# Optimization experiments

Hardware: AMD Instinct MI355X
Metric: run time of the kernel (lower is better)

Reference implementation:

```python
import jax, jax.numpy as jnp
import numpy as np

NUM_HEADS = 8
NORM_GROUPS = 32
EPS = 1e-5


def setup_inputs() -> dict:
    key = jax.random.key(0)
    k1, k2, k3 = jax.random.split(key, 3)
    b, c, h, w = 16, 256, 64, 64
    x = jax.random.normal(k1, (b, c, h, w), dtype=jnp.float32)
    gn_w = jnp.ones((c,), dtype=jnp.float32)
    gn_b = jnp.zeros((c,), dtype=jnp.float32)
    # 1x1 convs == channel matmuls; init like torch (kaiming-ish scale)
    w_qkv = jax.random.normal(k2, (3 * c, c), dtype=jnp.float32) / np.sqrt(c)
    w_proj = jax.random.normal(k3, (c, c), dtype=jnp.float32) / np.sqrt(c)
    b_proj = jnp.zeros((c,), dtype=jnp.float32)
    return {"x": x, "gn_w": gn_w, "gn_b": gn_b, "w_qkv": w_qkv,
            "w_proj": w_proj, "b_proj": b_proj}


def reference(x, gn_w, gn_b, w_qkv, w_proj, b_proj):
    b, c, h, w = x.shape
    H = NUM_HEADS
    d = c // H
    n = h * w
    # GroupNorm over (channels_per_group, h, w)
    xg = x.reshape(b, NORM_GROUPS, -1)
    mu = jnp.mean(xg, axis=-1, keepdims=True)
    var = jnp.mean(jnp.square(xg - mu), axis=-1, keepdims=True)
    xn = ((xg - mu) * jax.lax.rsqrt(var + EPS)).reshape(b, c, h, w)
    xn = xn * gn_w[None, :, None, None] + gn_b[None, :, None, None]
    # 1x1 conv -> (b, 3c, h, w); channel layout is (qkv, heads, d)
    qkv = jnp.einsum('oc,bchw->bohw', w_qkv, xn)
    qkv = qkv.reshape(b, 3, H, d, n)
    q, k, v = qkv[:, 0], qkv[:, 1], qkv[:, 2]  # each (b, H, d, n)
    k = jax.nn.softmax(k, axis=-1)
    # linear attention: small (d x d) state per head
    att = jnp.einsum('bhdn,bhen->bhde', k, v)
    out = jnp.einsum('bhde,bhdn->bhen', att, q)  # (b, H, d, n)
    out = out.reshape(b, c, h, w)
    return jnp.einsum('oc,bchw->bohw', w_proj, out) + b_proj[None, :, None, None]
```

## Files before the change

kernel.cpp:

```cpp
#include <hip/hip_runtime.h>
#include <stdint.h>

#define BATCH 16
#define CCH   256
#define NSP   4096

typedef unsigned short u16;
typedef short  short8 __attribute__((ext_vector_type(8)));
typedef float  f32x4  __attribute__((ext_vector_type(4)));

__device__ __forceinline__ float bf2f(u16 h) {
  union { unsigned int u; float f; } x; x.u = ((unsigned int)h) << 16; return x.f;
}
__device__ __forceinline__ u16 f2bf(float f) {
  union { float f; unsigned int u; } x; x.f = f;
  unsigned int r = 0x7fffu + ((x.u >> 16) & 1u);
  return (u16)((x.u + r) >> 16);
}

#define GLB(p) ((__attribute__((address_space(1))) void*)(p))
#define LDSP(p) ((__attribute__((address_space(3))) void*)(p))

__global__ __launch_bounds__(256) void prep_kernel(const float* __restrict__ x,
                                                   const float* __restrict__ wq,
                                                   const float* __restrict__ wp,
                                                   float2* __restrict__ stats,
                                                   float* __restrict__ att4,
                                                   u16* __restrict__ wbf,
                                                   u16* __restrict__ wqT) {
  __shared__ float red[8];
  __shared__ u16 ls[64][72];
  const int blk = blockIdx.x, tid = threadIdx.x;
  if (blk < 512) {
    {
      float* az = att4 + (size_t)blk * 264;
      for (int i = tid; i < 264; i += 256) az[i] = 0.f;
    }
    const float4* xv = (const float4*)(x + (size_t)blk * 32768);
    float s = 0.f, ss = 0.f;
    for (int i = tid; i < 8192; i += 256) {
      float4 u = xv[i];
      s  += u.x + u.y + u.z + u.w;
      ss += u.x * u.x + u.y * u.y + u.z * u.z + u.w * u.w;
    }
#pragma unroll
    for (int off = 32; off > 0; off >>= 1) {
      s  += __shfl_down(s, off);
      ss += __shfl_down(ss, off);
    }
    const int wave = tid >> 6, lane = tid & 63;
    if (lane == 0) { red[wave * 2] = s; red[wave * 2 + 1] = ss; }
    __syncthreads();
    if (tid == 0) {
      const float S  = red[0] + red[2] + red[4] + red[6];
      const float SS = red[1] + red[3] + red[5] + red[7];
      const float mean = S * (1.f / 32768.f);
      const float var  = SS * (1.f / 32768.f) - mean * mean;
      stats[blk] = make_float2(mean, rsqrtf(var + 1e-5f));
    }
  } else if (blk < 768) {
    const int i = ((blk - 512) * 256 + tid) * 4;
    float4 v = (i < 196608) ? *(const float4*)(wq + i)
                            : *(const float4*)(wp + (i - 196608));
    ushort4 o;
    o.x = f2bf(v.x); o.y = f2bf(v.y); o.z = f2bf(v.z); o.w = f2bf(v.w);
    *(ushort4*)(wbf + i) = o;
  } else {
    const int t2 = blk - 768;
    const int c0 = (t2 & 3) * 64, r0 = (t2 >> 2) * 64;
#pragma unroll
    for (int j = 0; j < 4; ++j) {
      const int row = j * 16 + (tid >> 4), col = (tid & 15) * 4;
      float4 u = *(const float4*)(wq + (r0 + row) * 256 + c0 + col);
      ls[row][col]     = f2bf(u.x);
      ls[row][col + 1] = f2bf(u.y);
      ls[row][col + 2] = f2bf(u.z);
      ls[row][col + 3] = f2bf(u.w);
    }
    __syncthreads();
#pragma unroll
    for (int j = 0; j < 2; ++j) {
      const int crow = j * 32 + (tid >> 3), d8 = (tid & 7) * 8;
      u16 tmp[8];
#pragma unroll
      for (int k = 0; k < 8; ++k) tmp[k] = ls[d8 + k][crow];
      *(uint4*)(wqT + (c0 + crow) * 256 + r0 + d8) = *(uint4*)tmp;
    }
  }
}

__global__ __launch_bounds__(256) void gn_apply_t(const float* __restrict__ x,
                                                  const float* __restrict__ gw,
                                                  const float* __restrict__ gb,
                                                  const float2* __restrict__ stats,
                                                  u16* __restrict__ xnT) {
  __shared__ u16 ls[64][72];
  const int b = blockIdx.z, c0 = blockIdx.y * 64, n0 = blockIdx.x * 64;
  const int tid = threadIdx.x;
#pragma unroll
  for (int r = 0; r < 4; ++r) {
    const int cc = (tid >> 4) + r * 16;
    const int nn = (tid & 15) * 4;
    const int c = c0 + cc;
    const float2 st = stats[b * 32 + (c >> 3)];
    const float wv = gw[c] * st.y;
    const float bv = gb[c] - st.x * wv;
    float4 u = *(const float4*)(x + ((size_t)b * CCH + c) * NSP + n0 + nn);
    ushort4 o;
    o.x = f2bf(u.x * wv + bv);
    o.y = f2bf(u.y * wv + bv);
    o.z = f2bf(u.z * wv + bv);
    o.w = f2bf(u.w * wv + bv);
    *(ushort4*)&ls[cc][nn] = o;
  }
  __syncthreads();
#pragma unroll
  for (int p = 0; p < 2; ++p) {
    const int idx = tid + p * 256;
    const int nn = idx >> 3;
    const int cb = (idx & 7) * 8;
    u16 tmp[8];
#pragma unroll
    for (int j = 0; j < 8; ++j) tmp[j] = ls[cb + j][nn];
    *(uint4*)(xnT + ((size_t)b * NSP + n0 + nn) * CCH + c0 + cb) = *(uint4*)tmp;
  }
}

__global__ __launch_bounds__(256) void gemm_f32(const u16* __restrict__ A,
                                                const u16* __restrict__ Bt,
                                                const float* __restrict__ bias,
                                                float* __restrict__ Cm, int M,
                                                int aBatch, long btStride, int ldc) {
  __shared__ __align__(16) u16 smem[17408];
  const int tid = threadIdx.x, wave = tid >> 6, lane = tid & 63;
  const int n0 = blockIdx.x * 128, m0 = blockIdx.y * 128, bz = blockIdx.z;
  const u16* Ab = A + (size_t)bz * aBatch;
  const u16* Bb = Bt + (size_t)bz * btStride;

  const int lrow = lane >> 3;
  const int kcl  = ((lane & 7) ^ lrow) * 8;
  const u16* pA[4]; const u16* pB[4];
#pragma unroll
  for (int j = 0; j < 4; ++j) {
    const int row = j * 32 + wave * 8 + lrow;
    pA[j] = Ab + (size_t)(m0 + row) * CCH + kcl;
    pB[j] = Bb + (size_t)(n0 + row) * CCH + kcl;
  }
  u16* lA = smem;
  u16* lB = smem + 8192;

  const int wm = wave >> 1, wn = wave & 1;
  f32x4 acc[4][4];
#pragma unroll
  for (int i = 0; i < 4; ++i)
#pragma unroll
    for (int j = 0; j < 4; ++j) acc[i][j] = (f32x4){0.f, 0.f, 0.f, 0.f};

  for (int it = 0; it < 4; ++it) {
#pragma unroll
    for (int j = 0; j < 4; ++j) {
      __builtin_amdgcn_global_load_lds(GLB(pA[j]), LDSP(lA + (j * 256 + wave * 64) * 8), 16, 0, 0);
      __builtin_amdgcn_global_load_lds(GLB(pB[j]), LDSP(lB + (j * 256 + wave * 64) * 8), 16, 0, 0);
      pA[j] += 64; pB[j] += 64;
    }
    __syncthreads();
#pragma unroll
    for (int w = 0; w < 2; ++w) {
      const int kcf = w * 4 + (lane >> 4);
      short8 af[4], bfr[4];
#pragma unroll
      for (int mt = 0; mt < 4; ++mt) {
        const int row = wm * 64 + mt * 16 + (lane & 15);
        af[mt] = *(const short8*)&lA[(row * 8 + (kcf ^ (row & 7))) * 8];
      }
#pragma unroll
      for (int nt = 0; nt < 4; ++nt) {
        const int row = wn * 64 + nt * 16 + (lane & 15);
        bfr[nt] = *(const short8*)&lB[(row * 8 + (kcf ^ (row & 7))) * 8];
      }
#pragma unroll
      for (int mt = 0; mt < 4; ++mt)
#pragma unroll
        for (int nt = 0; nt < 4; ++nt)
          acc[mt][nt] = __builtin_amdgcn_mfma_f32_16x16x32_bf16(af[mt], bfr[nt], acc[mt][nt], 0, 0, 0);
    }
    __syncthreads();
  }

  float* clf = (float*)smem;
  float* C = Cm + (size_t)bz * (size_t)M * ldc;
#pragma unroll
  for (int pass = 0; pass < 2; ++pass) {
    if (wm == pass) {
#pragma unroll
      for (int mt = 0; mt < 4; ++mt)
#pragma unroll
        for (int nt = 0; nt < 4; ++nt)
#pragma unroll
          for (int r = 0; r < 4; ++r) {
            const int rl = mt * 16 + (lane >> 4) * 4 + r;
            const int col = wn * 64 + nt * 16 + (lane & 15);
            clf[rl * 132 + col] = acc[mt][nt][r] + bias[m0 + pass * 64 + rl];
          }
    }
    __syncthreads();
#pragma unroll
    for (int j = 0; j < 8; ++j) {
      const int idx = tid + j * 256;
      const int row = idx >> 5, chunk = idx & 31;
      *(float4*)(C + (size_t)(m0 + pass * 64 + row) * ldc + n0 + chunk * 4) =
          *(const float4*)&clf[row * 132 + chunk * 4];
    }
    __syncthreads();
  }
}

__global__ __launch_bounds__(256, 4) void gemm_kv_att(const u16* __restrict__ A,
                                                      const u16* __restrict__ Bt,
                                                      float* __restrict__ att4) {
  __shared__ __align__(16) u16 smem[17408];
  const int tid = threadIdx.x, wave = tid >> 6, lane = tid & 63;
  const int n0 = blockIdx.x * 128, hg = blockIdx.y, b = blockIdx.z;
  const u16* Bb = Bt + (size_t)b * (size_t)NSP * CCH;

  const int lrow = lane >> 3;
  const int kcl  = ((lane & 7) ^ lrow) * 8;
  const u16* pA[4]; const u16* pB[4];
#pragma unroll
  for (int j = 0; j < 4; ++j) {
    const int arow = 256 + (j >> 1) * 256 + hg * 64 + (j & 1) * 32 + wave * 8 + lrow;
    pA[j] = A  + (size_t)arow * CCH + kcl;
    pB[j] = Bb + (size_t)(n0 + j * 32 + wave * 8 + lrow) * CCH + kcl;
  }
  u16* lA = smem;
  u16* lB = smem + 8192;

  const int wm = wave >> 1, wn = wave & 1;
  f32x4 acc[4][4];
#pragma unroll
  for (int i = 0; i < 4; ++i)
#pragma unroll
    for (int j = 0; j < 4; ++j) acc[i][j] = (f32x4){0.f, 0.f, 0.f, 0.f};

  for (int it = 0; it < 4; ++it) {
#pragma unroll
    for (int j = 0; j < 4; ++j) {
      __builtin_amdgcn_global_load_lds(GLB(pA[j]), LDSP(lA + (j * 256 + wave * 64) * 8), 16, 0, 0);
      __builtin_amdgcn_global_load_lds(GLB(pB[j]), LDSP(lB + (j * 256 + wave * 64) * 8), 16, 0, 0);
      pA[j] += 64; pB[j] += 64;
    }
    __syncthreads();
#pragma unroll
    for (int w = 0; w < 2; ++w) {
      const int kcf = w * 4 + (lane >> 4);
      short8 af[4], bfr[4];
#pragma unroll
      for (int mt = 0; mt < 4; ++mt) {
        const int row = wm * 64 + mt * 16 + (lane & 15);
        af[mt] = *(const short8*)&lA[(row * 8 + (kcf ^ (row & 7))) * 8];
      }
#pragma unroll
      for (int nt = 0; nt < 4; ++nt) {
        const int row = wn * 64 + nt * 16 + (lane & 15);
        bfr[nt] = *(const short8*)&lB[(row * 8 + (kcf ^ (row & 7))) * 8];
      }
#pragma unroll
      for (int mt = 0; mt < 4; ++mt)
#pragma unroll
        for (int nt = 0; nt < 4; ++nt)
          acc[mt][nt] = __builtin_amdgcn_mfma_f32_16x16x32_bf16(af[mt], bfr[nt], acc[mt][nt], 0, 0, 0);
    }
    __syncthreads();
  }

  u16* clK = smem;
  u16* clV = smem + 8704;
  {
    const int rbase = (lane >> 4) * 4;
    if (wm == 0) {
#pragma unroll
      for (int mt = 0; mt < 4; ++mt)
#pragma unroll
        for (int nt = 0; nt < 4; ++nt)
#pragma unroll
          for (int r = 0; r < 4; ++r) {
            const int row = mt * 16 + rbase + r;
            const int col = wn * 64 + nt * 16 + (lane & 15);
            clK[row * 136 + col] = f2bf(__expf(acc[mt][nt][r]));
          }
    } else {
#pragma unroll
      for (int mt = 0; mt < 4; ++mt)
#pragma unroll
        for (int nt = 0; nt < 4; ++nt)
#pragma unroll
          for (int r = 0; r < 4; ++r) {
            const int row = mt * 16 + rbase + r;
            const int col = wn * 64 + nt * 16 + (lane & 15);
            clV[row * 136 + col] = f2bf(acc[mt][nt][r]);
          }
    }
  }
  __syncthreads();

  const int hh = wave >> 1, nhalf = wave & 1;
  const int bh = b * 8 + hg * 2 + hh;
  f32x4 a2[2][2], al[2];
#pragma unroll
  for (int i = 0; i < 2; ++i) {
    al[i] = (f32x4){0.f, 0.f, 0.f, 0.f};
#pragma unroll
    for (int j = 0; j < 2; ++j) a2[i][j] = (f32x4){0.f, 0.f, 0.f, 0.f};
  }
  short8 ones;
#pragma unroll
  for (int j = 0; j < 8; ++j) ones[j] = (short)0x3F80;

  const int rr = lane & 15, cc8 = (lane >> 4) * 8;
#pragma unroll
  for (int c = 0; c < 2; ++c) {
    const int n = (nhalf * 2 + c) * 32 + cc8;
    short8 ek0 = *(const short8*)&clK[(hh * 32 + rr) * 136 + n];
    short8 ek1 = *(const short8*)&clK[(hh * 32 + 16 + rr) * 136 + n];
    short8 v0  = *(const short8*)&clV[(hh * 32 + rr) * 136 + n];
    short8 v1  = *(const short8*)&clV[(hh * 32 + 16 + rr) * 136 + n];
    a2[0][0] = __builtin_amdgcn_mfma_f32_16x16x32_bf16(ek0, v0, a2[0][0], 0, 0, 0);
    a2[0][1] = __builtin_amdgcn_mfma_f32_16x16x32_bf16(ek0, v1, a2[0][1], 0, 0, 0);
    a2[1][0] = __builtin_amdgcn_mfma_f32_16x16x32_bf16(ek1, v0, a2[1][0], 0, 0, 0);
    a2[1][1] = __builtin_amdgcn_mfma_f32_16x16x32_bf16(ek1, v1, a2[1][1], 0, 0, 0);
    al[0]    = __builtin_amdgcn_mfma_f32_16x16x32_bf16(ek0, ones, al[0], 0, 0, 0);
    al[1]    = __builtin_amdgcn_mfma_f32_16x16x32_bf16(ek1, ones, al[1], 0, 0, 0);
  }
  __syncthreads();

  float* red  = (float*)smem;
  float* redl = red + 2176;
  const int dq = (lane >> 4) * 4;
  if (nhalf == 1) {
#pragma unroll
    for (int dh = 0; dh < 2; ++dh) {
#pragma unroll
      for (int eh = 0; eh < 2; ++eh)
#pragma unroll
        for (int j = 0; j < 4; ++j)
          red[hh * 1088 + (dh * 16 + dq + j) * 34 + eh * 16 + rr] = a2[dh][eh][j];
      if (rr == 0)
#pragma unroll
        for (int j = 0; j < 4; ++j) redl[hh * 32 + dh * 16 + dq + j] = al[dh][j];
    }
  }
  __syncthreads();
  if (nhalf == 0) {
    float* ap = att4 + (size_t)bh * 1056;
#pragma unroll
    for (int dh = 0; dh < 2; ++dh) {
#pragma unroll
      for (int eh = 0; eh < 2; ++eh)
#pragma unroll
        for (int j = 0; j < 4; ++j) {
          const int d = dh * 16 + dq + j, e = eh * 16 + rr;
          atomicAdd(&ap[d * 32 + e], a2[dh][eh][j] + red[hh * 1088 + d * 34 + e]);
        }
      if (rr == 0)
#pragma unroll
        for (int j = 0; j < 4; ++j) {
          const int d = dh * 16 + dq + j;
          atomicAdd(&ap[1024 + d], al[dh][j] + redl[hh * 32 + d]);
        }
    }
  }
}

__global__ __launch_bounds__(256) void w23_kernel(const u16* __restrict__ wp_bf,
                                                  const u16* __restrict__ wqT,
                                                  const float* __restrict__ att4,
                                                  u16* __restrict__ W3) {
  __shared__ __align__(16) u16 smem[58880];
  const int tid = threadIdx.x, wave = tid >> 6, lane = tid & 63;
  const int n0 = blockIdx.x * 128, m0 = blockIdx.y * 128, b = blockIdx.z;

  u16*   lA  = smem;
  float* asb = (float*)(smem + 33792);
  u16*   lB  = smem + 50688;

  {
    const float* ab = att4 + (size_t)b * 8 * 1056;
    for (int i = tid; i < 8192; i += 256) {
      const int h = i >> 10, d = (i >> 5) & 31, e = i & 31;
      asb[h * 1056 + d * 33 + e] = ab[h * 1056 + d * 32 + e] / ab[h * 1056 + 1024 + d];
    }
  }
  __syncthreads();

  {
    const int r16 = lane & 15, e0 = (lane >> 4) * 8;
#pragma unroll
    for (int hh = 0; hh < 2; ++hh) {
      const int h = wave * 2 + hh;
#pragma unroll
      for (int nt = 0; nt < 2; ++nt) {
        const float* bp = asb + h * 1056 + (nt * 16 + r16) * 33 + e0;
        short8 bfr;
#pragma unroll
        for (int j = 0; j < 8; ++j) bfr[j] = (short)f2bf(bp[j]);
#pragma unroll
        for (int mt = 0; mt < 8; ++mt) {
          const int orow = mt * 16 + r16;
          short8 af = *(const short8*)(wp_bf + (size_t)(m0 + orow) * 256 + h * 32 + e0);
          f32x4 c = __builtin_amdgcn_mfma_f32_16x16x32_bf16(af, bfr, (f32x4){0.f,0.f,0.f,0.f}, 0, 0, 0);
#pragma unroll
          for (int r = 0; r < 4; ++r) {
            const int o = mt * 16 + (lane >> 4) * 4 + r;
            const int d2 = h * 32 + nt * 16 + r16;
            lA[o * 264 + d2] = f2bf(c[r]);
          }
        }
      }
    }
  }
  __syncthreads();

  const int lrow = lane >> 3;
  const int kcl  = ((lane & 7) ^ lrow) * 8;
  const u16* pB[4];
#pragma unroll
  for (int j = 0; j < 4; ++j)
    pB[j] = wqT + (size_t)(n0 + j * 32 + wave * 8 + lrow) * 256 + kcl;

  const int wm = wave >> 1, wn = wave & 1;
  f32x4 acc[4][4];
#pragma unroll
  for (int i = 0; i < 4; ++i)
#pragma unroll
    for (int j = 0; j < 4; ++j) acc[i][j] = (f32x4){0.f, 0.f, 0.f, 0.f};

  for (int it = 0; it < 4; ++it) {
#pragma unroll
    for (int j = 0; j < 4; ++j) {
      __builtin_amdgcn_global_load_lds(GLB(pB[j]), LDSP(lB + (j * 256 + wave * 64) * 8), 16, 0, 0);
      pB[j] += 64;
    }
    __syncthreads();
#pragma unroll
    for (int w = 0; w < 2; ++w) {
      const int kcf = w * 4 + (lane >> 4);
      short8 af[4], bfr[4];
#pragma unroll
      for (int mt = 0; mt < 4; ++mt) {
        const int row = wm * 64 + mt * 16 + (lane & 15);
        af[mt] = *(const short8*)&lA[row * 264 + it * 64 + kcf * 8];
      }
#pragma unroll
      for (int nt = 0; nt < 4; ++nt) {
        const int row = wn * 64 + nt * 16 + (lane & 15);
        bfr[nt] = *(const short8*)&lB[(row * 8 + (kcf ^ (row & 7))) * 8];
      }
#pragma unroll
      for (int mt = 0; mt < 4; ++mt)
#pragma unroll
        for (int nt = 0; nt < 4; ++nt)
          acc[mt][nt] = __builtin_amdgcn_mfma_f32_16x16x32_bf16(af[mt], bfr[nt], acc[mt][nt], 0, 0, 0);
    }
    __syncthreads();
  }

  u16* cl = smem + 33792;
#pragma unroll
  for (int mt = 0; mt < 4; ++mt)
#pragma unroll
    for (int nt = 0; nt < 4; ++nt)
#pragma unroll
      for (int r = 0; r < 4; ++r) {
        const int row = wm * 64 + mt * 16 + (lane >> 4) * 4 + r;
        const int col = wn * 64 + nt * 16 + (lane & 15);
        cl[row * 136 + col] = f2bf(acc[mt][nt][r]);
      }
  __syncthreads();
  u16* C = W3 + (size_t)b * 65536;
#pragma unroll
  for (int j = 0; j < 8; ++j) {
    const int idx = tid + j * 256;
    const int row = idx >> 4, chunk = idx & 15;
    *(uint4*)(C + (size_t)(m0 + row) * 256 + n0 + chunk * 8) =
        *(const uint4*)&cl[row * 136 + chunk * 8];
  }
}

extern "C" void kernel_launch(void* const* d_in, const int* in_sizes, int n_in,
                              void* d_out, int out_size, void* d_ws, size_t ws_size,
                              hipStream_t stream) {
  const float* x      = (const float*)d_in[0];
  const float* gn_w   = (const float*)d_in[1];
  const float* gn_b   = (const float*)d_in[2];
  const float* w_qkv  = (const float*)d_in[3];
  const float* w_proj = (const float*)d_in[4];
  const float* b_proj = (const float*)d_in[5];
  float* out = (float*)d_out;

  char* ws = (char*)d_ws;
  u16*    xnT   = (u16*)ws;
  u16*    wbf   = (u16*)(ws + 33554432ull);
  u16*    wqT   = (u16*)(ws + 34078720ull);
  u16*    W3    = (u16*)(ws + 36306944ull);
  float*  att4  = (float*)(ws + 38404096ull);
  float2* stats = (float2*)(ws + 38944768ull);
  u16* wq_bf = wbf;
  u16* wp_bf = wbf + 196608;

  prep_kernel<<<784, 256, 0, stream>>>(x, w_qkv, w_proj, stats, att4, wbf, wqT);
  gn_apply_t<<<dim3(64, 4, 16), 256, 0, stream>>>(x, gn_w, gn_b, stats, xnT);
  gemm_kv_att<<<dim3(32, 4, 16), 256, 0, stream>>>(wq_bf, xnT, att4);
  w23_kernel<<<dim3(2, 2, 16), 256, 0, stream>>>(wp_bf, wqT, att4, W3);
  gemm_f32<<<dim3(32, 2, 16), 256, 0, stream>>>(W3, xnT, b_proj, out,
                                                CCH, 65536, (long)NSP * CCH, NSP);
}
```

Before: 214.3 us.

## Fold GroupNorm affine into per-batch weights and fuse stats with x transpose

Drops the separate GroupNorm stats pass and normalized-activation pass. The x transpose/bf16 cast now accumulates group sums via atomics in the same read. The normalization scale and shift are folded algebraically into per-batch KV weights, Q bias and the W3 column scaling, so x is read once instead of twice. This adds a per-batch weight-fold kernel and a memset. It also uses atomics and a single-pass variance (E[x²]−mean²), and feeds raw rather than normalized activations into bf16.

```diff
diff --git a/kernel.cpp b/kernel.cpp
--- a/kernel.cpp
+++ b/kernel.cpp
@@ -21,52 +21,59 @@
 #define GLB(p) ((__attribute__((address_space(1))) void*)(p))
 #define LDSP(p) ((__attribute__((address_space(3))) void*)(p))
 
-__global__ __launch_bounds__(256) void prep_kernel(const float* __restrict__ x,
-                                                   const float* __restrict__ wq,
-                                                   const float* __restrict__ wp,
-                                                   float2* __restrict__ stats,
-                                                   float* __restrict__ att4,
-                                                   u16* __restrict__ wbf,
-                                                   u16* __restrict__ wqT) {
-  __shared__ float red[8];
+__global__ __launch_bounds__(256) void xprep_kernel(const float* __restrict__ x,
+                                                    const float* __restrict__ wq,
+                                                    const float* __restrict__ wp,
+                                                    u16* __restrict__ xT,
+                                                    u16* __restrict__ wpbf,
+                                                    u16* __restrict__ wqT,
+                                                    float* __restrict__ att4,
+                                                    float* __restrict__ gstat) {
   __shared__ u16 ls[64][72];
   const int blk = blockIdx.x, tid = threadIdx.x;
-  if (blk < 512) {
-    {
-      float* az = att4 + (size_t)blk * 264;
-      for (int i = tid; i < 264; i += 256) az[i] = 0.f;
-    }
-    const float4* xv = (const float4*)(x + (size_t)blk * 32768);
+  if (blk < 4096) {
+    const int n0 = (blk & 63) * 64, c0 = ((blk >> 6) & 3) * 64, b = blk >> 8;
+    const int q = tid >> 4, nn = (tid & 15) * 4;
     float s = 0.f, ss = 0.f;
-    for (int i = tid; i < 8192; i += 256) {
-      float4 u = xv[i];
+#pragma unroll
+    for (int r = 0; r < 4; ++r) {
+      const int cc = q * 4 + r;
+      float4 u = *(const float4*)(x + ((size_t)b * CCH + c0 + cc) * NSP + n0 + nn);
+      ushort4 o;
+      o.x = f2bf(u.x); o.y = f2bf(u.y); o.z = f2bf(u.z); o.w = f2bf(u.w);
+      *(ushort4*)&ls[cc][nn] = o;
       s  += u.x + u.y + u.z + u.w;
       ss += u.x * u.x + u.y * u.y + u.z * u.z + u.w * u.w;
     }
 #pragma unroll
-    for (int off = 32; off > 0; off >>= 1) {
-      s  += __shfl_down(s, off);
-      ss += __shfl_down(ss, off);
-    }
-    const int wave = tid >> 6, lane = tid & 63;
-    if (lane == 0) { red[wave * 2] = s; red[wave * 2 + 1] = ss; }
-    __syncthreads();
-    if (tid == 0) {
-      const float S  = red[0] + red[2] + red[4] + red[6];
-      const float SS = red[1] + red[3] + red[5] + red[7];
-      const float mean = S * (1.f / 32768.f);
-      const float var  = SS * (1.f / 32768.f) - mean * mean;
-      stats[blk] = make_float2(mean, rsqrtf(var + 1e-5f));
-    }
-  } else if (blk < 768) {
-    const int i = ((blk - 512) * 256 + tid) * 4;
-    float4 v = (i < 196608) ? *(const float4*)(wq + i)
-                            : *(const float4*)(wp + (i - 196608));
+    for (int m = 16; m >= 1; m >>= 1) {
+      s  += __shfl_xor(s, m);
+      ss += __shfl_xor(ss, m);
+    }
+    if ((tid & 31) == 0) {
+      const int g = ((blk >> 6) & 3) * 8 + (q >> 1);
+      atomicAdd(&gstat[(b * 32 + g) * 2 + 0], s);
+      atomicAdd(&gstat[(b * 32 + g) * 2 + 1], ss);
+    }
+    __syncthreads();
+#pragma unroll
+    for (int p = 0; p < 2; ++p) {
+      const int idx = tid + p * 256;
+      const int nnr = idx >> 3;
+      const int cb = (idx & 7) * 8;
+      u16 tmp[8];
+#pragma unroll
+      for (int j = 0; j < 8; ++j) tmp[j] = ls[cb + j][nnr];
+      *(uint4*)(xT + ((size_t)b * NSP + n0 + nnr) * CCH + c0 + cb) = *(uint4*)tmp;
+    }
+  } else if (blk < 4160) {
+    const int i = ((blk - 4096) * 256 + tid) * 4;
+    float4 v = *(const float4*)(wp + i);
     ushort4 o;
     o.x = f2bf(v.x); o.y = f2bf(v.y); o.z = f2bf(v.z); o.w = f2bf(v.w);
-    *(ushort4*)(wbf + i) = o;
-  } else {
-    const int t2 = blk - 768;
+    *(ushort4*)(wpbf + i) = o;
+  } else if (blk < 4176) {
+    const int t2 = blk - 4160;
     const int c0 = (t2 & 3) * 64, r0 = (t2 >> 2) * 64;
 #pragma unroll
     for (int j = 0; j < 4; ++j) {
@@ -86,65 +93,85 @@
       for (int k = 0; k < 8; ++k) tmp[k] = ls[d8 + k][crow];
       *(uint4*)(wqT + (c0 + crow) * 256 + r0 + d8) = *(uint4*)tmp;
     }
-  }
-}
-
-__global__ __launch_bounds__(256) void gn_apply_t(const float* __restrict__ x,
-                                                  const float* __restrict__ gw,
-                                                  const float* __restrict__ gb,
-                                                  const float2* __restrict__ stats,
-                                                  u16* __restrict__ xnT) {
-  __shared__ u16 ls[64][72];
-  const int b = blockIdx.z, c0 = blockIdx.y * 64, n0 = blockIdx.x * 64;
+  } else {
+    float4 z = {0.f, 0.f, 0.f, 0.f};
+    *(float4*)(att4 + (size_t)(blk - 4176) * 1024 + tid * 4) = z;
+  }
+}
+
+__global__ __launch_bounds__(256) void wfold_kernel(const float* __restrict__ wqkv,
+                                                    const float* __restrict__ gw,
+                                                    const float* __restrict__ gb,
+                                                    const float* __restrict__ gstat,
+                                                    u16* __restrict__ Akv,
+                                                    float* __restrict__ wvv_g,
+                                                    float* __restrict__ qbias,
+                                                    float* __restrict__ kvbias) {
+  __shared__ float wvv[256], bvv[256];
+  const int rt = blockIdx.x, b = blockIdx.y;
   const int tid = threadIdx.x;
-#pragma unroll
-  for (int r = 0; r < 4; ++r) {
-    const int cc = (tid >> 4) + r * 16;
-    const int nn = (tid & 15) * 4;
-    const int c = c0 + cc;
-    const float2 st = stats[b * 32 + (c >> 3)];
-    const float wv = gw[c] * st.y;
-    const float bv = gb[c] - st.x * wv;
-    float4 u = *(const float4*)(x + ((size_t)b * CCH + c) * NSP + n0 + nn);
-    ushort4 o;
-    o.x = f2bf(u.x * wv + bv);
-    o.y = f2bf(u.y * wv + bv);
-    o.z = f2bf(u.z * wv + bv);
-    o.w = f2bf(u.w * wv + bv);
-    *(ushort4*)&ls[cc][nn] = o;
-  }
-  __syncthreads();
-#pragma unroll
-  for (int p = 0; p < 2; ++p) {
-    const int idx = tid + p * 256;
-    const int nn = idx >> 3;
-    const int cb = (idx & 7) * 8;
-    u16 tmp[8];
-#pragma unroll
-    for (int j = 0; j < 8; ++j) tmp[j] = ls[cb + j][nn];
-    *(uint4*)(xnT + ((size_t)b * NSP + n0 + nn) * CCH + c0 + cb) = *(uint4*)tmp;
-  }
-}
-
-__global__ __launch_bounds__(256) void gemm_f32(const u16* __restrict__ A,
-                                                const u16* __restrict__ Bt,
-                                                const float* __restrict__ bias,
-                                                float* __restrict__ Cm, int M,
-                                                int aBatch, long btStride, int ldc) {
+  if (tid < 32) {
+    const float gs  = gstat[(b * 32 + tid) * 2 + 0];
+    const float gss = gstat[(b * 32 + tid) * 2 + 1];
+    const float mean = gs * (1.f / 32768.f);
+    const float var  = gss * (1.f / 32768.f) - mean * mean;
+    const float rs = rsqrtf(var + 1e-5f);
+#pragma unroll
+    for (int j = 0; j < 8; ++j) {
+      const int c = tid * 8 + j;
+      const float wv = gw[c] * rs;
+      wvv[c] = wv;
+      bvv[c] = gb[c] - mean * wv;
+      if (rt == 0) wvv_g[b * 256 + c] = wv;
+    }
+  }
+  __syncthreads();
+  const int row_l = tid >> 3, k = tid & 7, c0 = k * 32;
+  const int grow = rt * 32 + row_l;
+  const float* wr = wqkv + (size_t)grow * 256 + c0;
+  float acc = 0.f;
+  u16 ob[32];
+#pragma unroll
+  for (int jj = 0; jj < 8; ++jj) {
+    float4 u = *(const float4*)(wr + jj * 4);
+    const float* uf = (const float*)&u;
+#pragma unroll
+    for (int t = 0; t < 4; ++t) {
+      const int c = c0 + jj * 4 + t;
+      acc += uf[t] * bvv[c];
+      ob[jj * 4 + t] = f2bf(uf[t] * wvv[c]);
+    }
+  }
+#pragma unroll
+  for (int m = 4; m >= 1; m >>= 1) acc += __shfl_xor(acc, m);
+  if (grow < 256) {
+    if (k == 0) qbias[b * 256 + grow] = acc;
+  } else {
+    u16* dst = Akv + ((size_t)b * 512 + grow - 256) * 256 + c0;
+#pragma unroll
+    for (int j = 0; j < 4; ++j) ((uint4*)dst)[j] = ((const uint4*)ob)[j];
+    if (k == 0) kvbias[b * 512 + grow - 256] = acc;
+  }
+}
+
+__global__ __launch_bounds__(256, 4) void gemm_kv_att(const u16* __restrict__ Akv,
+                                                      const u16* __restrict__ Bt,
+                                                      const float* __restrict__ kvbias,
+                                                      float* __restrict__ att4) {
   __shared__ __align__(16) u16 smem[17408];
   const int tid = threadIdx.x, wave = tid >> 6, lane = tid & 63;
-  const int n0 = blockIdx.x * 128, m0 = blockIdx.y * 128, bz = blockIdx.z;
-  const u16* Ab = A + (size_t)bz * aBatch;
-  const u16* Bb = Bt + (size_t)bz * btStride;
+  const int n0 = blockIdx.x * 128, hg = blockIdx.y, b = blockIdx.z;
+  const u16* Ab = Akv + (size_t)b * 512 * 256;
+  const u16* Bb = Bt + (size_t)b * (size_t)NSP * CCH;
 
   const int lrow = lane >> 3;
   const int kcl  = ((lane & 7) ^ lrow) * 8;
   const u16* pA[4]; const u16* pB[4];
 #pragma unroll
   for (int j = 0; j < 4; ++j) {
-    const int row = j * 32 + wave * 8 + lrow;
-    pA[j] = Ab + (size_t)(m0 + row) * CCH + kcl;
-    pB[j] = Bb + (size_t)(n0 + row) * CCH + kcl;
+    const int arow = (j >> 1) * 256 + hg * 64 + (j & 1) * 32 + wave * 8 + lrow;
+    pA[j] = Ab + (size_t)arow * CCH + kcl;
+    pB[j] = Bb + (size_t)(n0 + j * 32 + wave * 8 + lrow) * CCH + kcl;
   }
   u16* lA = smem;
   u16* lB = smem + 8192;
@@ -187,96 +214,11 @@
     __syncthreads();
   }
 
-  float* clf = (float*)smem;
-  float* C = Cm + (size_t)bz * (size_t)M * ldc;
-#pragma unroll
-  for (int pass = 0; pass < 2; ++pass) {
-    if (wm == pass) {
-#pragma unroll
-      for (int mt = 0; mt < 4; ++mt)
-#pragma unroll
-        for (int nt = 0; nt < 4; ++nt)
-#pragma unroll
-          for (int r = 0; r < 4; ++r) {
-            const int rl = mt * 16 + (lane >> 4) * 4 + r;
-            const int col = wn * 64 + nt * 16 + (lane & 15);
-            clf[rl * 132 + col] = acc[mt][nt][r] + bias[m0 + pass * 64 + rl];
-          }
-    }
-    __syncthreads();
-#pragma unroll
-    for (int j = 0; j < 8; ++j) {
-      const int idx = tid + j * 256;
-      const int row = idx >> 5, chunk = idx & 31;
-      *(float4*)(C + (size_t)(m0 + pass * 64 + row) * ldc + n0 + chunk * 4) =
-          *(const float4*)&clf[row * 132 + chunk * 4];
-    }
-    __syncthreads();
-  }
-}
-
-__global__ __launch_bounds__(256, 4) void gemm_kv_att(const u16* __restrict__ A,
-                                                      const u16* __restrict__ Bt,
-                                                      float* __restrict__ att4) {
-  __shared__ __align__(16) u16 smem[17408];
-  const int tid = threadIdx.x, wave = tid >> 6, lane = tid & 63;
-  const int n0 = blockIdx.x * 128, hg = blockIdx.y, b = blockIdx.z;
-  const u16* Bb = Bt + (size_t)b * (size_t)NSP * CCH;
-
-  const int lrow = lane >> 3;
-  const int kcl  = ((lane & 7) ^ lrow) * 8;
-  const u16* pA[4]; const u16* pB[4];
-#pragma unroll
-  for (int j = 0; j < 4; ++j) {
-    const int arow = 256 + (j >> 1) * 256 + hg * 64 + (j & 1) * 32 + wave * 8 + lrow;
-    pA[j] = A  + (size_t)arow * CCH + kcl;
-    pB[j] = Bb + (size_t)(n0 + j * 32 + wave * 8 + lrow) * CCH + kcl;
-  }
-  u16* lA = smem;
-  u16* lB = smem + 8192;
-
-  const int wm = wave >> 1, wn = wave & 1;
-  f32x4 acc[4][4];
-#pragma unroll
-  for (int i = 0; i < 4; ++i)
-#pragma unroll
-    for (int j = 0; j < 4; ++j) acc[i][j] = (f32x4){0.f, 0.f, 0.f, 0.f};
-
-  for (int it = 0; it < 4; ++it) {
-#pragma unroll
-    for (int j = 0; j < 4; ++j) {
-      __builtin_amdgcn_global_load_lds(GLB(pA[j]), LDSP(lA + (j * 256 + wave * 64) * 8), 16, 0, 0);
-      __builtin_amdgcn_global_load_lds(GLB(pB[j]), LDSP(lB + (j * 256 + wave * 64) * 8), 16, 0, 0);
-      pA[j] += 64; pB[j] += 64;
-    }
-    __syncthreads();
-#pragma unroll
-    for (int w = 0; w < 2; ++w) {
-      const int kcf = w * 4 + (lane >> 4);
-      short8 af[4], bfr[4];
-#pragma unroll
-      for (int mt = 0; mt < 4; ++mt) {
-        const int row = wm * 64 + mt * 16 + (lane & 15);
-        af[mt] = *(const short8*)&lA[(row * 8 + (kcf ^ (row & 7))) * 8];
-      }
-#pragma unroll
-      for (int nt = 0; nt < 4; ++nt) {
-        const int row = wn * 64 + nt * 16 + (lane & 15);
-        bfr[nt] = *(const short8*)&lB[(row * 8 + (kcf ^ (row & 7))) * 8];
-      }
-#pragma unroll
-      for (int mt = 0; mt < 4; ++mt)
-#pragma unroll
-        for (int nt = 0; nt < 4; ++nt)
-          acc[mt][nt] = __builtin_amdgcn_mfma_f32_16x16x32_bf16(af[mt], bfr[nt], acc[mt][nt], 0, 0, 0);
-    }
-    __syncthreads();
-  }
-
   u16* clK = smem;
   u16* clV = smem + 8704;
   {
     const int rbase = (lane >> 4) * 4;
+    const float* kb = kvbias + b * 512 + (wm ? 256 : 0) + hg * 64;
     if (wm == 0) {
 #pragma unroll
       for (int mt = 0; mt < 4; ++mt)
@@ -286,7 +228,7 @@
           for (int r = 0; r < 4; ++r) {
             const int row = mt * 16 + rbase + r;
             const int col = wn * 64 + nt * 16 + (lane & 15);
-            clK[row * 136 + col] = f2bf(__expf(acc[mt][nt][r]));
+            clK[row * 136 + col] = f2bf(__expf(acc[mt][nt][r] + kb[row]));
           }
     } else {
 #pragma unroll
@@ -297,7 +239,7 @@
           for (int r = 0; r < 4; ++r) {
             const int row = mt * 16 + rbase + r;
             const int col = wn * 64 + nt * 16 + (lane & 15);
-            clV[row * 136 + col] = f2bf(acc[mt][nt][r]);
+            clV[row * 136 + col] = f2bf(acc[mt][nt][r] + kb[row]);
           }
     }
   }
@@ -374,7 +316,11 @@
 __global__ __launch_bounds__(256) void w23_kernel(const u16* __restrict__ wp_bf,
                                                   const u16* __restrict__ wqT,
                                                   const float* __restrict__ att4,
-                                                  u16* __restrict__ W3) {
+                                                  const float* __restrict__ wvv_g,
+                                                  const float* __restrict__ qbias,
+                                                  const float* __restrict__ bproj,
+                                                  u16* __restrict__ W3,
+                                                  float* __restrict__ bias3) {
   __shared__ __align__(16) u16 smem[58880];
   const int tid = threadIdx.x, wave = tid >> 6, lane = tid & 63;
   const int n0 = blockIdx.x * 128, m0 = blockIdx.y * 128, b = blockIdx.z;
@@ -420,6 +366,17 @@
   }
   __syncthreads();
 
+  if (blockIdx.x == 0) {
+    const int row = tid >> 1, half = tid & 1;
+    const float* qb = qbias + b * 256 + half * 128;
+    const u16* la = lA + row * 264 + half * 128;
+    float s = 0.f;
+#pragma unroll
+    for (int d = 0; d < 128; ++d) s += bf2f(la[d]) * qb[d];
+    s += __shfl_xor(s, 1);
+    if (half == 0) bias3[b * 256 + m0 + row] = s + bproj[m0 + row];
+  }
+
   const int lrow = lane >> 3;
   const int kcl  = ((lane & 7) ^ lrow) * 8;
   const u16* pB[4];
@@ -466,15 +423,17 @@
 
   u16* cl = smem + 33792;
 #pragma unroll
-  for (int mt = 0; mt < 4; ++mt)
-#pragma unroll
-    for (int nt = 0; nt < 4; ++nt)
+  for (int nt = 0; nt < 4; ++nt) {
+    const int col = wn * 64 + nt * 16 + (lane & 15);
+    const float wvc = wvv_g[b * 256 + n0 + col];
+#pragma unroll
+    for (int mt = 0; mt < 4; ++mt)
 #pragma unroll
       for (int r = 0; r < 4; ++r) {
         const int row = wm * 64 + mt * 16 + (lane >> 4) * 4 + r;
-        const int col = wn * 64 + nt * 16 + (lane & 15);
-        cl[row * 136 + col] = f2bf(acc[mt][nt][r]);
-      }
+        cl[row * 136 + col] = f2bf(acc[mt][nt][r] * wvc);
+      }
+  }
   __syncthreads();
   u16* C = W3 + (size_t)b * 65536;
 #pragma unroll
@@ -483,6 +442,94 @@
     const int row = idx >> 4, chunk = idx & 15;
     *(uint4*)(C + (size_t)(m0 + row) * 256 + n0 + chunk * 8) =
         *(const uint4*)&cl[row * 136 + chunk * 8];
+  }
+}
+
+__global__ __launch_bounds__(256) void gemm_f32(const u16* __restrict__ A,
+                                                const u16* __restrict__ Bt,
+                                                const float* __restrict__ bias3,
+                                                float* __restrict__ Cm) {
+  __shared__ __align__(16) u16 smem[17408];
+  const int tid = threadIdx.x, wave = tid >> 6, lane = tid & 63;
+  const int n0 = blockIdx.x * 128, m0 = blockIdx.y * 128, bz = blockIdx.z;
+  const u16* Ab = A + (size_t)bz * 65536;
+  const u16* Bb = Bt + (size_t)bz * (size_t)NSP * CCH;
+
+  const int lrow = lane >> 3;
+  const int kcl  = ((lane & 7) ^ lrow) * 8;
+  const u16* pA[4]; const u16* pB[4];
+#pragma unroll
+  for (int j = 0; j < 4; ++j) {
+    const int row = j * 32 + wave * 8 + lrow;
+    pA[j] = Ab + (size_t)(m0 + row) * CCH + kcl;
+    pB[j] = Bb + (size_t)(n0 + row) * CCH + kcl;
+  }
+  u16* lA = smem;
+  u16* lB = smem + 8192;
+
+  const int wm = wave >> 1, wn = wave & 1;
+  f32x4 acc[4][4];
+#pragma unroll
+  for (int i = 0; i < 4; ++i)
+#pragma unroll
+    for (int j = 0; j < 4; ++j) acc[i][j] = (f32x4){0.f, 0.f, 0.f, 0.f};
+
+  for (int it = 0; it < 4; ++it) {
+#pragma unroll
+    for (int j = 0; j < 4; ++j) {
+      __builtin_amdgcn_global_load_lds(GLB(pA[j]), LDSP(lA + (j * 256 + wave * 64) * 8), 16, 0, 0);
+      __builtin_amdgcn_global_load_lds(GLB(pB[j]), LDSP(lB + (j * 256 + wave * 64) * 8), 16, 0, 0);
+      pA[j] += 64; pB[j] += 64;
+    }
+    __syncthreads();
+#pragma unroll
+    for (int w = 0; w < 2; ++w) {
+      const int kcf = w * 4 + (lane >> 4);
+      short8 af[4], bfr[4];
+#pragma unroll
+      for (int mt = 0; mt < 4; ++mt) {
+        const int row = wm * 64 + mt * 16 + (lane & 15);
+        af[mt] = *(const short8*)&lA[(row * 8 + (kcf ^ (row & 7))) * 8];
+      }
+#pragma unroll
+      for (int nt = 0; nt < 4; ++nt) {
+        const int row = wn * 64 + nt * 16 + (lane & 15);
+        bfr[nt] = *(const short8*)&lB[(row * 8 + (kcf ^ (row & 7))) * 8];
+      }
+#pragma unroll
+      for (int mt = 0; mt < 4; ++mt)
+#pragma unroll
+        for (int nt = 0; nt < 4; ++nt)
+          acc[mt][nt] = __builtin_amdgcn_mfma_f32_16x16x32_bf16(af[mt], bfr[nt], acc[mt][nt], 0, 0, 0);
+    }
+    __syncthreads();
+  }
+
+  float* clf = (float*)smem;
+  float* C = Cm + (size_t)bz * (size_t)CCH * NSP;
+#pragma unroll
+  for (int pass = 0; pass < 2; ++pass) {
+    if (wm == pass) {
+#pragma unroll
+      for (int mt = 0; mt < 4; ++mt)
+#pragma unroll
+        for (int nt = 0; nt < 4; ++nt)
+#pragma unroll
+          for (int r = 0; r < 4; ++r) {
+            const int rl = mt * 16 + (lane >> 4) * 4 + r;
+            const int col = wn * 64 + nt * 16 + (lane & 15);
+            clf[rl * 132 + col] = acc[mt][nt][r] + bias3[bz * 256 + m0 + pass * 64 + rl];
+          }
+    }
+    __syncthreads();
+#pragma unroll
+    for (int j = 0; j < 8; ++j) {
+      const int idx = tid + j * 256;
+      const int row = idx >> 5, chunk = idx & 31;
+      *(float4*)(C + (size_t)(m0 + pass * 64 + row) * NSP + n0 + chunk * 4) =
+          *(const float4*)&clf[row * 132 + chunk * 4];
+    }
+    __syncthreads();
   }
 }
 
@@ -498,19 +545,24 @@
   float* out = (float*)d_out;
 
   char* ws = (char*)d_ws;
-  u16*    xnT   = (u16*)ws;
-  u16*    wbf   = (u16*)(ws + 33554432ull);
-  u16*    wqT   = (u16*)(ws + 34078720ull);
-  u16*    W3    = (u16*)(ws + 36306944ull);
-  float*  att4  = (float*)(ws + 38404096ull);
-  float2* stats = (float2*)(ws + 38944768ull);
-  u16* wq_bf = wbf;
-  u16* wp_bf = wbf + 196608;
-
-  prep_kernel<<<784, 256, 0, stream>>>(x, w_qkv, w_proj, stats, att4, wbf, wqT);
-  gn_apply_t<<<dim3(64, 4, 16), 256, 0, stream>>>(x, gn_w, gn_b, stats, xnT);
-  gemm_kv_att<<<dim3(32, 4, 16), 256, 0, stream>>>(wq_bf, xnT, att4);
-  w23_kernel<<<dim3(2, 2, 16), 256, 0, stream>>>(wp_bf, wqT, att4, W3);
-  gemm_f32<<<dim3(32, 2, 16), 256, 0, stream>>>(W3, xnT, b_proj, out,
-                                                CCH, 65536, (long)NSP * CCH, NSP);
-}
+  u16*   xT     = (u16*)ws;
+  u16*   wpbf   = (u16*)(ws + 33554432ull);
+  u16*   wqT    = (u16*)(ws + 33685504ull);
+  u16*   Akv    = (u16*)(ws + 33816576ull);
+  u16*   W3     = (u16*)(ws + 38010880ull);
+  float* att4   = (float*)(ws + 40108032ull);
+  float* gstat  = (float*)(ws + 40648704ull);
+  float* wvv_g  = (float*)(ws + 40652800ull);
+  float* qbias  = (float*)(ws + 40669184ull);
+  float* kvbias = (float*)(ws + 40685568ull);
+  float* bias3  = (float*)(ws + 40718336ull);
+
+  hipMemsetAsync(gstat, 0, 4096, stream);
+  xprep_kernel<<<4308, 256, 0, stream>>>(x, w_qkv, w_proj, xT, wpbf, wqT, att4, gstat);
+  wfold_kernel<<<dim3(24, 16), 256, 0, stream>>>(w_qkv, gn_w, gn_b, gstat,
+                                                 Akv, wvv_g, qbias, kvbias);
+  gemm_kv_att<<<dim3(32, 4, 16), 256, 0, stream>>>(Akv, xT, kvbias, att4);
+  w23_kernel<<<dim3(2, 2, 16), 256, 0, stream>>>(wpbf, wqT, att4, wvv_g, qbias,
+                                                 b_proj, W3, bias3);
+  gemm_f32<<<dim3(32, 2, 16), 256, 0, stream>>>(W3, xT, bias3, out);
+}
```

After: 208.7 us. -2.6%, faster.
